# Kernel optimization log

Hardware: AMD Instinct MI355X
Metric: run time of the kernel (lower is better)

The kernel has to match this reference:

```python
import jax, jax.numpy as jnp
import numpy as np

B, N, E = 4096, 32, 64
IN_DIM, H = 74, 256
ADD_DIM = 2
MLP1, MLP2 = 1024, 512
GCR_LAYERS = 5


def setup_inputs() -> dict:
    key = jax.random.key(0)
    ks = jax.random.split(key, 26)
    s = 0.05
    inp = {
        "x": jax.random.normal(ks[0], (B, N, IN_DIM), jnp.float32),
        "add_features": jax.random.normal(ks[1], (B, ADD_DIM), jnp.float32),
        "src": jax.random.randint(ks[2], (B, E), 0, N, jnp.int32),
        "dst": jax.random.randint(ks[3], (B, E), 0, N, jnp.int32),
        # first GraphConv (in_dim -> hidden)
        "W_in": jax.random.normal(ks[4], (IN_DIM, H), jnp.float32) * s,
        "b_in": jnp.zeros((H,), jnp.float32),
        # 5 GCR blocks, each with two GraphConv layers (hidden -> hidden)
        "W_g1": jax.random.normal(ks[5], (GCR_LAYERS, H, H), jnp.float32) * s,
        "b_g1": jnp.zeros((GCR_LAYERS, H), jnp.float32),
        "W_g2": jax.random.normal(ks[6], (GCR_LAYERS, H, H), jnp.float32) * s,
        "b_g2": jnp.zeros((GCR_LAYERS, H), jnp.float32),
        # attention pooling
        "Wq": jax.random.normal(ks[7], (H, H), jnp.float32) * s,
        "bq": jnp.zeros((H,), jnp.float32),
        "Wk": jax.random.normal(ks[8], (H, H), jnp.float32) * s,
        "bk": jnp.zeros((H,), jnp.float32),
        "Wv": jax.random.normal(ks[9], (H, 1), jnp.float32) * s,
        "bv": jnp.zeros((1,), jnp.float32),
        "W_m1": jax.random.normal(ks[10], (H + ADD_DIM, MLP1), jnp.float32) * s,
        "b_m1": jnp.zeros((MLP1,), jnp.float32),
        "W_m2": jax.random.normal(ks[11], (MLP1, MLP2), jnp.float32) * s,
        "b_m2": jnp.zeros((MLP2,), jnp.float32),
        "W_m3": jax.random.normal(ks[12], (MLP2, 1), jnp.float32) * s,
        "b_m3": jnp.zeros((1,), jnp.float32),
    }
    return inp


def _forward(x, add_features, src, dst, W_in, b_in, W_g1, b_g1, W_g2, b_g2,
             Wq, bq, Wk, bk, Wv, bv, W_m1, b_m1, W_m2, b_m2, W_m3, b_m3):
    def per_graph(xg, sg, dg):
        # DGL GraphConv norm='both': D_out^{-1/2} on src side, D_in^{-1/2} on dst side
        ones = jnp.ones((E,), xg.dtype)
        out_deg = jnp.zeros((N,), xg.dtype).at[sg].add(ones)
        in_deg = jnp.zeros((N,), xg.dtype).at[dg].add(ones)
        onorm = jax.lax.rsqrt(jnp.clip(out_deg, 1.0))
        inorm = jax.lax.rsqrt(jnp.clip(in_deg, 1.0))

        def conv(h, W, b):
            h = (h * onorm[:, None]) @ W                      # [N, out]
            agg = jnp.zeros((N, W.shape[1]), h.dtype).at[dg].add(h[sg])
            return agg * inorm[:, None] + b

        h = conv(xg, W_in, b_in)
        for i in range(GCR_LAYERS):
            t = conv(h, W_g1[i], b_g1[i])
            t = conv(jax.nn.relu(t), W_g2[i], b_g2[i])
            h = jax.nn.relu(t)                                # GCR output (res_connection=0)
        # attention-weighted pooling over nodes
        q = h @ Wq + bq                                       # [N, H]
        k = h @ Wk + bk                                       # [N, H]
        v = h @ Wv + bv                                       # [N, 1]
        attn = jax.nn.softmax(q @ k.T, axis=1)                # [N, N]
        w = (attn @ v)[:, 0]                                  # [N]
        return h.T @ w                                        # [H]

    feats = jax.vmap(per_graph)(x, src, dst)                  # [B, H]
    z = jnp.concatenate([feats, add_features], axis=1)        # [B, H+ADD_DIM]
    z = jax.nn.leaky_relu(z @ W_m1 + b_m1)
    z = jax.nn.leaky_relu(z @ W_m2 + b_m2)
    z = z @ W_m3 + b_m3                                       # [B, 1]
    return z[:, 0]


def reference(x, add_features, src, dst, W_in, b_in, W_g1, b_g1, W_g2, b_g2,
              Wq, bq, Wk, bk, Wv, bv, W_m1, b_m1, W_m2, b_m2, W_m3, b_m3):
    return _forward(x, add_features, src, dst, W_in, b_in, W_g1, b_g1, W_g2, b_g2,
                    Wq, bq, Wk, bk, Wv, bv, W_m1, b_m1, W_m2, b_m2, W_m3, b_m3)
```

## Files before the change

kernel.cpp:

```cpp
#include <hip/hip_runtime.h>
#include <math.h>

#define BB     4096
#define NN     32
#define EE     64
#define INDIM  74
#define HH     256
#define GCR    5
#define M1     1024
#define M2     512
#define FDIM   258
#define ADDD   2
#define FSTR   288

typedef __attribute__((ext_vector_type(8))) _Float16 half8_t;
typedef __attribute__((ext_vector_type(4))) float float4_t;

#define MF16(a, b, c) __builtin_amdgcn_mfma_f32_16x16x32_f16((a), (b), (c), 0, 0, 0)
#define LO_SCALE 1024.0f

#define WS_FH     0
#define WS_WQK    4227072
#define WS_TVEC   4489216
#define WS_PK     4490240
#define PK_WIN_HI 0
#define PK_WIN_LO 24576
#define PK_G_BASE 49152
#define PK_G_STRIDE 131072
#define PK_WQK_HI 1359872
#define PK_WQK_LO (1359872 + 65536)
#define PK_W1P    1490944
#define PK_W2P    1785856

union H4 { unsigned long long u; _Float16 h[4]; };

__global__ void prep1_kernel(const float* __restrict__ Wq, const float* __restrict__ Wk,
                             const float* __restrict__ bq,
                             float* __restrict__ wqkf, float* __restrict__ tvec) {
  const int i = blockIdx.x, j = threadIdx.x;
  if (i < 256) {
    __shared__ float qrow[256];
    qrow[j] = Wq[i * 256 + j];
    __syncthreads();
    float s = 0.f;
    for (int c = 0; c < 256; ++c) s = fmaf(qrow[c], Wk[j * 256 + c], s);
    wqkf[i * 256 + j] = s;
  } else {
    float s = 0.f;
    for (int c = 0; c < 256; ++c) s = fmaf(Wk[j * 256 + c], bq[c], s);
    tvec[j] = s;
  }
}

template<int KS, int KREAL>
__device__ __forceinline__ void pack_one(const float* __restrict__ S,
                                         _Float16* __restrict__ hi,
                                         _Float16* __restrict__ lo, int local) {
  const int l = local & 63;
  const int nk = local >> 6;
  const int ks = nk % KS;
  const int nt = nk / KS;
  const int j = nt * 16 + (l & 15);
  const int kbase = ks * 32 + (l >> 4) * 8;
  half8_t h8, l8;
  #pragma unroll
  for (int i = 0; i < 8; ++i) {
    const int k = kbase + i;
    const float v = (k < KREAL) ? S[k * 256 + j] : 0.f;
    const _Float16 hb = (_Float16)v;
    h8[i] = hb;
    l8[i] = (_Float16)((v - (float)hb) * LO_SCALE);
  }
  *(half8_t*)(hi + (size_t)local * 8) = h8;
  *(half8_t*)(lo + (size_t)local * 8) = l8;
}

__global__ void prep2_kernel(const float* __restrict__ W_in,
                             const float* __restrict__ W_g1, const float* __restrict__ W_g2,
                             const float* __restrict__ wqkf, _Float16* __restrict__ pk) {
  const int cid = blockIdx.x * 256 + threadIdx.x;
  if (cid < 3072) {
    pack_one<3, 74>(W_in, pk + PK_WIN_HI, pk + PK_WIN_LO, cid);
  } else {
    const int m = (cid - 3072) >> 13;
    const int local = (cid - 3072) & 8191;
    _Float16* hi; const float* S;
    if (m < 10) {
      hi = pk + PK_G_BASE + (size_t)m * PK_G_STRIDE;
      S = (m < 5) ? (W_g1 + (size_t)m * 65536) : (W_g2 + (size_t)(m - 5) * 65536);
    } else {
      hi = pk + PK_WQK_HI;
      S = wqkf;
    }
    pack_one<8, 256>(S, hi, hi + 65536, local);
  }
}

template<int KS, int KREAL, int NCOL>
__device__ __forceinline__ void pack_flat(const float* __restrict__ S,
                                          _Float16* __restrict__ dst, int local) {
  const int l = local & 63;
  const int nk = local >> 6;
  const int ks = nk % KS;
  const int nt = nk / KS;
  const int j = nt * 16 + (l & 15);
  const int kbase = ks * 32 + (l >> 4) * 8;
  half8_t h8;
  #pragma unroll
  for (int i = 0; i < 8; ++i) {
    const int k = kbase + i;
    h8[i] = (_Float16)((k < KREAL) ? S[(size_t)k * NCOL + j] : 0.f);
  }
  *(half8_t*)(dst + (size_t)local * 8) = h8;
}

__global__ void prep3_kernel(const float* __restrict__ W1, const float* __restrict__ W2,
                             _Float16* __restrict__ pk) {
  const int cid = blockIdx.x * 256 + threadIdx.x;
  if (cid < 36864) {
    pack_flat<9, 258, 1024>(W1, pk + PK_W1P, cid);
  } else {
    pack_flat<32, 1024, 512>(W2, pk + PK_W2P, cid - 36864);
  }
}

template<int KS, bool RELU>
__device__ __forceinline__ void conv2x(
    _Float16* Hs, _Float16* Tb,
    const half8_t nm[2][2],
    const _Float16* __restrict__ Whi,
    const float* __restrict__ bias,
    int lane, int wv)
{
  const int g4 = lane >> 4, l15 = lane & 15;
  const int sw = l15 << 3;

  float4_t th[2][2][2];
  #pragma unroll
  for (int a = 0; a < 2; ++a)
    #pragma unroll
    for (int b = 0; b < 2; ++b)
      #pragma unroll
      for (int c = 0; c < 2; ++c)
        th[a][b][c] = (float4_t){0.f, 0.f, 0.f, 0.f};

  #pragma unroll
  for (int ks = 0; ks < KS; ++ks) {
    const half8_t wh0 = *(const half8_t*)(Whi + ((wv * KS + ks) * 64 + lane) * 8);
    const half8_t wh1 = *(const half8_t*)(Whi + (((8 + wv) * KS + ks) * 64 + lane) * 8);
    const int j0 = ks * 32 + g4 * 8;
    #pragma unroll
    for (int gi = 0; gi < 2; ++gi)
      #pragma unroll
      for (int mt = 0; mt < 2; ++mt) {
        const half8_t ha = *(const half8_t*)(Hs + (gi << 13) + ((mt * 16 + l15) * 256 + (j0 ^ sw)));
        th[0][gi][mt] = MF16(ha, wh0, th[0][gi][mt]);
        th[1][gi][mt] = MF16(ha, wh1, th[1][gi][mt]);
      }
  }

  #pragma unroll
  for (int ni = 0; ni < 2; ++ni) {
    const int nt = ni * 8 + wv;
    #pragma unroll
    for (int gi = 0; gi < 2; ++gi)
      #pragma unroll
      for (int mt = 0; mt < 2; ++mt) {
        const int r0 = mt * 16 + 4 * g4;
        H4 pk4;
        #pragma unroll
        for (int jj = 0; jj < 4; ++jj)
          pk4.h[jj] = (_Float16)th[ni][gi][mt][jj];
        const int idx = nt * 512 + ((r0 >> 3) * 16 + l15) * 8 + (r0 & 7);
        *(unsigned long long*)(Tb + (gi << 13) + idx) = pk4.u;
      }
  }

  __syncthreads();

  #pragma unroll
  for (int ni = 0; ni < 2; ++ni) {
    const int nt = ni * 8 + wv;
    const float4 b4 = *(const float4*)&bias[nt * 16 + 4 * g4];
    const int j0 = nt * 16 + 4 * g4;
    #pragma unroll
    for (int gi = 0; gi < 2; ++gi) {
      const half8_t ta = *(const half8_t*)(Tb + (gi << 13) + nt * 512 + lane * 8);
      #pragma unroll
      for (int nt2 = 0; nt2 < 2; ++nt2) {
        const float4_t dh = MF16(ta, nm[gi][nt2], ((float4_t){0.f, 0.f, 0.f, 0.f}));
        H4 pk4;
        #pragma unroll
        for (int jj = 0; jj < 4; ++jj) {
          float v = dh[jj] + ((const float*)&b4)[jj];
          if (RELU) v = fmaxf(v, 0.f);
          pk4.h[jj] = (_Float16)v;
        }
        const int n = nt2 * 16 + l15;
        *(unsigned long long*)(Hs + (gi << 13) + (n * 256 + (j0 ^ ((n & 15) << 3)))) = pk4.u;
      }
    }
  }
  __syncthreads();
}

__global__ __launch_bounds__(512, 4)
void gnn_kernel(const float* __restrict__ x, const float* __restrict__ addf,
                const int* __restrict__ src, const int* __restrict__ dst,
                const float* __restrict__ b_in,
                const float* __restrict__ b_g1, const float* __restrict__ b_g2,
                const float* __restrict__ Wvp, const float* __restrict__ bv,
                const _Float16* __restrict__ pk,
                const float* __restrict__ tvec,
                _Float16* __restrict__ Fh)
{
  __shared__ __align__(16) _Float16 Hs[2][8192];
  __shared__ __align__(16) _Float16 Tb[2][8192];
  __shared__ float Sb[2][1184];

  const int tid = threadIdx.x;
  const int lane = tid & 63;
  const int wv = tid >> 6;
  const int g4 = lane >> 4, l15 = lane & 15;
  const int sw = l15 << 3;
  const int ga = blockIdx.x * 2;

  for (int i = tid; i < 2048; i += 512) Sb[i >> 10][i & 1023] = 0.f;
  __syncthreads();
  if (tid < 128) {
    const int gi = tid >> 6, e = tid & 63;
    const int es = src[(size_t)(ga + gi) * EE + e];
    const int ed = dst[(size_t)(ga + gi) * EE + e];
    atomicAdd(&Sb[gi][ed * 32 + es], 1.0f);
  }
  __syncthreads();
  if (tid < 64) {
    const int gi = tid >> 5, n = tid & 31;
    float s = 0.f;
    for (int m = 0; m < NN; ++m) s += Sb[gi][n * 32 + m];
    Sb[gi][1056 + n] = 1.f / sqrtf(fmaxf(s, 1.f));
  } else if (tid < 128) {
    const int gi = (tid - 64) >> 5, n = tid & 31;
    float s = 0.f;
    for (int m = 0; m < NN; ++m) s += Sb[gi][m * 32 + n];
    Sb[gi][1088 + n] = 1.f / sqrtf(fmaxf(s, 1.f));
  }
  __syncthreads();
  for (int i = tid; i < 2048; i += 512) {
    const int gi = i >> 10, idx = i & 1023;
    Sb[gi][idx] *= Sb[gi][1056 + (idx >> 5)] * Sb[gi][1088 + (idx & 31)];
  }
  __syncthreads();

  half8_t nm[2][2];
  #pragma unroll
  for (int gi = 0; gi < 2; ++gi)
    #pragma unroll
    for (int nt2 = 0; nt2 < 2; ++nt2)
      #pragma unroll
      for (int i = 0; i < 8; ++i)
        nm[gi][nt2][i] = (_Float16)Sb[gi][(nt2 * 16 + l15) * 32 + g4 * 8 + i];

  for (int i = tid; i < 2 * NN * 96; i += 512) {
    const int gi = i / 3072, rem = i - gi * 3072;
    const int r = rem / 96, c = rem - r * 96;
    const float vx = (c < INDIM) ? x[(size_t)(ga + gi) * (NN * INDIM) + r * INDIM + c] : 0.f;
    Hs[gi][r * 256 + (c ^ ((r & 15) << 3))] = (_Float16)vx;
  }
  __syncthreads();

  conv2x<3, false>(&Hs[0][0], &Tb[0][0], nm, pk + PK_WIN_HI, b_in, lane, wv);
  #pragma unroll 1
  for (int L = 0; L < GCR; ++L) {
    conv2x<8, true>(&Hs[0][0], &Tb[0][0], nm,
                    pk + PK_G_BASE + (size_t)L * PK_G_STRIDE, b_g1 + L * HH, lane, wv);
    conv2x<8, true>(&Hs[0][0], &Tb[0][0], nm,
                    pk + PK_G_BASE + (size_t)(5 + L) * PK_G_STRIDE, b_g2 + L * HH, lane, wv);
  }

  {
    const _Float16* Qhi = pk + PK_WQK_HI;
    const int sgi = wv >> 2, smt = (wv >> 1) & 1, snt = wv & 1;

    float4_t uh[2][2][2];
    #pragma unroll
    for (int a = 0; a < 2; ++a)
      #pragma unroll
      for (int b = 0; b < 2; ++b)
        #pragma unroll
        for (int c = 0; c < 2; ++c)
          uh[a][b][c] = (float4_t){0.f, 0.f, 0.f, 0.f};

    #pragma unroll
    for (int ks = 0; ks < 8; ++ks) {
      const half8_t qh0 = *(const half8_t*)(Qhi + ((wv * 8 + ks) * 64 + lane) * 8);
      const half8_t qh1 = *(const half8_t*)(Qhi + (((8 + wv) * 8 + ks) * 64 + lane) * 8);
      const int j0 = ks * 32 + g4 * 8;
      #pragma unroll
      for (int gi = 0; gi < 2; ++gi)
        #pragma unroll
        for (int mt = 0; mt < 2; ++mt) {
          const half8_t ha = *(const half8_t*)(&Hs[gi][(mt * 16 + l15) * 256 + (j0 ^ sw)]);
          uh[0][gi][mt] = MF16(ha, qh0, uh[0][gi][mt]);
          uh[1][gi][mt] = MF16(ha, qh1, uh[1][gi][mt]);
        }
    }
    #pragma unroll
    for (int ni = 0; ni < 2; ++ni) {
      const int nt = ni * 8 + wv;
      const float tv = tvec[nt * 16 + l15];
      const int cl = nt * 16 + l15;
      #pragma unroll
      for (int gi = 0; gi < 2; ++gi)
        #pragma unroll
        for (int mt = 0; mt < 2; ++mt)
          #pragma unroll
          for (int jj = 0; jj < 4; ++jj) {
            const int n = mt * 16 + 4 * g4 + jj;
            Tb[gi][n * 256 + (cl ^ ((n & 15) << 3))] =
                (_Float16)(uh[ni][gi][mt][jj] + tv);
          }
    }
    __syncthreads();
    float4_t sacc = (float4_t){0.f, 0.f, 0.f, 0.f};
    #pragma unroll
    for (int ksl = 0; ksl < 8; ++ksl) {
      const int kl = ksl * 32 + g4 * 8;
      const half8_t ua = *(const half8_t*)(&Tb[sgi][(smt * 16 + l15) * 256 + (kl ^ sw)]);
      const half8_t hb = *(const half8_t*)(&Hs[sgi][(snt * 16 + l15) * 256 + (kl ^ sw)]);
      sacc = MF16(ua, hb, sacc);
    }
    #pragma unroll
    for (int jj = 0; jj < 4; ++jj)
      Sb[sgi][(smt * 16 + 4 * g4 + jj) * 33 + snt * 16 + l15] = sacc[jj];
  }

  {
    const int gi = tid >> 8, m = (tid >> 3) & 31, q = tid & 7;
    float s = 0.f;
    const int c0 = q * 32;
    for (int cc = 0; cc < 32; ++cc) {
      const int c = c0 + cc;
      s = fmaf((float)Hs[gi][m * 256 + (c ^ ((m & 15) << 3))], Wvp[c], s);
    }
    s += __shfl_xor(s, 1);
    s += __shfl_xor(s, 2);
    s += __shfl_xor(s, 4);
    if (q == 0) Sb[gi][1120 + m] = s + bv[0];
  }
  __syncthreads();

  if (tid < 64) {
    const int gi = tid >> 5, n = tid & 31;
    float mx = -1e30f;
    #pragma unroll 1
    for (int m = 0; m < NN; ++m) mx = fmaxf(mx, Sb[gi][n * 33 + m]);
    float se = 0.f, sv = 0.f;
    #pragma unroll 1
    for (int m = 0; m < NN; ++m) {
      const float e = expf(Sb[gi][n * 33 + m] - mx);
      se += e;
      sv = fmaf(e, Sb[gi][1120 + m], sv);
    }
    Sb[gi][1152 + n] = sv / se;
  }
  __syncthreads();

  {
    const int gi = tid >> 8, j = tid & 255;
    float f0 = 0.f;
    #pragma unroll
    for (int m = 0; m < NN; ++m) {
      const float w = Sb[gi][1152 + m];
      f0 = fmaf((float)Hs[gi][m * 256 + (j ^ ((m & 15) << 3))], w, f0);
    }
    Fh[(size_t)(ga + gi) * FSTR + j] = (_Float16)f0;
    if (tid < 64) {
      const int g2 = tid >> 5, c = 256 + (tid & 31);
      Fh[(size_t)(ga + g2) * FSTR + c] =
          (c < FDIM) ? (_Float16)addf[(size_t)(ga + g2) * ADDD + (c - 256)] : (_Float16)0.f;
    }
  }
}

__global__ __launch_bounds__(512, 4)
void mlp_kernel(const _Float16* __restrict__ Fh,
                const _Float16* __restrict__ W1p, const float* __restrict__ b1,
                const _Float16* __restrict__ W2p, const float* __restrict__ b2,
                const float* __restrict__ W3, const float* __restrict__ b3,
                float* __restrict__ out)
{
  __shared__ __align__(16) _Float16 Ft[16 * 320];
  __shared__ __align__(16) _Float16 Z1[16 * 1024];
  __shared__ __align__(16) _Float16 Z2[16 * 512];

  const int tid = threadIdx.x, lane = tid & 63, wv = tid >> 6;
  const int g4 = lane >> 4, l15 = lane & 15;
  const int sw = (l15 & 7) << 3;
  const int r0 = blockIdx.x * 16;

  for (int i = tid; i < 16 * FSTR; i += 512) {
    const int r = i / FSTR, c = i - r * FSTR;
    Ft[r * 320 + (c ^ ((r & 7) << 3))] = Fh[(size_t)(r0 + r) * FSTR + c];
  }
  __syncthreads();

  {
    float4_t a1[8];
    #pragma unroll
    for (int t = 0; t < 8; ++t) a1[t] = (float4_t){0.f, 0.f, 0.f, 0.f};
    #pragma unroll
    for (int ks = 0; ks < 9; ++ks) {
      const half8_t fb = *(const half8_t*)(Ft + l15 * 320 + ((ks * 32 + g4 * 8) ^ sw));
      #pragma unroll
      for (int t = 0; t < 8; ++t) {
        const int jt = wv * 8 + t;
        const half8_t wf = *(const half8_t*)(W1p + ((size_t)(jt * 9 + ks) * 64 + lane) * 8);
        a1[t] = MF16(wf, fb, a1[t]);
      }
    }
    #pragma unroll
    for (int t = 0; t < 8; ++t) {
      const int j0 = (wv * 8 + t) * 16 + 4 * g4;
      const float4 bb = *(const float4*)&b1[j0];
      H4 pk4;
      #pragma unroll
      for (int jj = 0; jj < 4; ++jj) {
        const float z = a1[t][jj] + ((const float*)&bb)[jj];
        pk4.h[jj] = (_Float16)fmaxf(z, 0.01f * z);
      }
      *(unsigned long long*)(Z1 + l15 * 1024 + (j0 ^ sw)) = pk4.u;
    }
  }
  __syncthreads();

  {
    float4_t a2[4];
    #pragma unroll
    for (int t = 0; t < 4; ++t) a2[t] = (float4_t){0.f, 0.f, 0.f, 0.f};
    #pragma unroll 4
    for (int ks = 0; ks < 32; ++ks) {
      const half8_t zb = *(const half8_t*)(Z1 + l15 * 1024 + ((ks * 32 + g4 * 8) ^ sw));
      #pragma unroll
      for (int t = 0; t < 4; ++t) {
        const int jt = wv * 4 + t;
        const half8_t wf = *(const half8_t*)(W2p + ((size_t)(jt * 32 + ks) * 64 + lane) * 8);
        a2[t] = MF16(wf, zb, a2[t]);
      }
    }
    #pragma unroll
    for (int t = 0; t < 4; ++t) {
      const int j0 = (wv * 4 + t) * 16 + 4 * g4;
      const float4 bb = *(const float4*)&b2[j0];
      H4 pk4;
      #pragma unroll
      for (int jj = 0; jj < 4; ++jj) {
        const float z = a2[t][jj] + ((const float*)&bb)[jj];
        pk4.h[jj] = (_Float16)fmaxf(z, 0.01f * z);
      }
      *(unsigned long long*)(Z2 + l15 * 512 + (j0 ^ sw)) = pk4.u;
    }
  }
  __syncthreads();

  {
    const int m = tid >> 5, q = tid & 31;
    const int swm = (m & 7) << 3;
    float s = 0.f;
    #pragma unroll
    for (int h = 0; h < 2; ++h) {
      const int c0 = q * 16 + h * 8;
      const half8_t z8 = *(const half8_t*)(Z2 + m * 512 + (c0 ^ swm));
      #pragma unroll
      for (int i2 = 0; i2 < 8; ++i2)
        s = fmaf((float)z8[i2], W3[c0 + i2], s);
    }
    s += __shfl_xor(s, 1);
    s += __shfl_xor(s, 2);
    s += __shfl_xor(s, 4);
    s += __shfl_xor(s, 8);
    s += __shfl_xor(s, 16);
    if (q == 0) out[r0 + m] = s + b3[0];
  }
}

extern "C" void kernel_launch(void* const* d_in, const int* in_sizes, int n_in,
                              void* d_out, int out_size, void* d_ws, size_t ws_size,
                              hipStream_t stream) {
  (void)in_sizes; (void)n_in; (void)out_size; (void)ws_size;
  const float* x    = (const float*)d_in[0];
  const float* addf = (const float*)d_in[1];
  const int*   src  = (const int*)d_in[2];
  const int*   dst  = (const int*)d_in[3];
  const float* W_in = (const float*)d_in[4];
  const float* b_in = (const float*)d_in[5];
  const float* W_g1 = (const float*)d_in[6];
  const float* b_g1 = (const float*)d_in[7];
  const float* W_g2 = (const float*)d_in[8];
  const float* b_g2 = (const float*)d_in[9];
  const float* Wq   = (const float*)d_in[10];
  const float* bq   = (const float*)d_in[11];
  const float* Wk   = (const float*)d_in[12];
  const float* Wv   = (const float*)d_in[14];
  const float* bv   = (const float*)d_in[15];
  const float* W1   = (const float*)d_in[16];
  const float* b1   = (const float*)d_in[17];
  const float* W2   = (const float*)d_in[18];
  const float* b2   = (const float*)d_in[19];
  const float* W3   = (const float*)d_in[20];
  const float* b3   = (const float*)d_in[21];
  float* out = (float*)d_out;

  _Float16* Fh    = (_Float16*)((char*)d_ws + WS_FH);
  float* wqkf     = (float*)((char*)d_ws + WS_WQK);
  float* tvec     = (float*)((char*)d_ws + WS_TVEC);
  _Float16* pk    = (_Float16*)((char*)d_ws + WS_PK);

  prep1_kernel<<<dim3(257), dim3(256), 0, stream>>>(Wq, Wk, bq, wqkf, tvec);
  prep2_kernel<<<dim3(364), dim3(256), 0, stream>>>(W_in, W_g1, W_g2, wqkf, pk);
  prep3_kernel<<<dim3(400), dim3(256), 0, stream>>>(W1, W2, pk);
  gnn_kernel<<<dim3(BB / 2), dim3(512), 0, stream>>>(
      x, addf, src, dst, b_in, b_g1, b_g2, Wv, bv, pk, tvec, Fh);
  mlp_kernel<<<dim3(BB / 16), dim3(512), 0, stream>>>(
      Fh, pk + PK_W1P, b1, pk + PK_W2P, b2, W3, b3, out);
}
```

Before: 341.4 us.

## Switch GNN conv layers to 32x32x16 MFMA with per-wave column tiles

Rewrites the graph-conv and Q·K projection stages to use 32x32x16 f16 MFMA, so each wave owns a 32-column slice across all 32 nodes instead of two 16-column tiles. The weight packing is changed to match the new fragment layout, and the unused lo-part packing is dropped. The aggregation step now uses per-wave transposed scratch with a new swizzle. The aim is fewer MFMA issues and LDS fragment loads per layer. In exchange, accumulator register pressure rises, and the new LDS swizzles could introduce bank conflicts.

```diff
diff --git a/kernel.cpp b/kernel.cpp
--- a/kernel.cpp
+++ b/kernel.cpp
@@ -15,24 +15,30 @@
 
 typedef __attribute__((ext_vector_type(8))) _Float16 half8_t;
 typedef __attribute__((ext_vector_type(4))) float float4_t;
+typedef __attribute__((ext_vector_type(16))) float float16_t;
 
 #define MF16(a, b, c) __builtin_amdgcn_mfma_f32_16x16x32_f16((a), (b), (c), 0, 0, 0)
-#define LO_SCALE 1024.0f
+#define MF32(a, b, c) __builtin_amdgcn_mfma_f32_32x32x16_f16((a), (b), (c), 0, 0, 0)
 
 #define WS_FH     0
 #define WS_WQK    4227072
 #define WS_TVEC   4489216
 #define WS_PK     4490240
 #define PK_WIN_HI 0
-#define PK_WIN_LO 24576
 #define PK_G_BASE 49152
 #define PK_G_STRIDE 131072
 #define PK_WQK_HI 1359872
-#define PK_WQK_LO (1359872 + 65536)
 #define PK_W1P    1490944
 #define PK_W2P    1785856
 
 union H4 { unsigned long long u; _Float16 h[4]; };
+
+__device__ __forceinline__ float16_t zero16() {
+  float16_t z;
+  #pragma unroll
+  for (int e = 0; e < 16; ++e) z[e] = 0.f;
+  return z;
+}
 
 __global__ void prep1_kernel(const float* __restrict__ Wq, const float* __restrict__ Wk,
                              const float* __restrict__ bq,
@@ -52,27 +58,22 @@
   }
 }
 
-template<int KS, int KREAL>
-__device__ __forceinline__ void pack_one(const float* __restrict__ S,
-                                         _Float16* __restrict__ hi,
-                                         _Float16* __restrict__ lo, int local) {
+template<int KS16, int KREAL>
+__device__ __forceinline__ void pack32(const float* __restrict__ S,
+                                       _Float16* __restrict__ dst, int local) {
   const int l = local & 63;
   const int nk = local >> 6;
-  const int ks = nk % KS;
-  const int nt = nk / KS;
-  const int j = nt * 16 + (l & 15);
-  const int kbase = ks * 32 + (l >> 4) * 8;
-  half8_t h8, l8;
+  const int ks = nk % KS16;
+  const int nt = nk / KS16;
+  const int j = nt * 32 + (l & 31);
+  const int kbase = ks * 16 + (l >> 5) * 8;
+  half8_t h8;
   #pragma unroll
   for (int i = 0; i < 8; ++i) {
     const int k = kbase + i;
-    const float v = (k < KREAL) ? S[k * 256 + j] : 0.f;
-    const _Float16 hb = (_Float16)v;
-    h8[i] = hb;
-    l8[i] = (_Float16)((v - (float)hb) * LO_SCALE);
-  }
-  *(half8_t*)(hi + (size_t)local * 8) = h8;
-  *(half8_t*)(lo + (size_t)local * 8) = l8;
+    h8[i] = (_Float16)((k < KREAL) ? S[k * 256 + j] : 0.f);
+  }
+  *(half8_t*)(dst + (size_t)local * 8) = h8;
 }
 
 __global__ void prep2_kernel(const float* __restrict__ W_in,
@@ -80,19 +81,16 @@
                              const float* __restrict__ wqkf, _Float16* __restrict__ pk) {
   const int cid = blockIdx.x * 256 + threadIdx.x;
   if (cid < 3072) {
-    pack_one<3, 74>(W_in, pk + PK_WIN_HI, pk + PK_WIN_LO, cid);
+    pack32<6, 74>(W_in, pk + PK_WIN_HI, cid);
   } else {
     const int m = (cid - 3072) >> 13;
     const int local = (cid - 3072) & 8191;
-    _Float16* hi; const float* S;
     if (m < 10) {
-      hi = pk + PK_G_BASE + (size_t)m * PK_G_STRIDE;
-      S = (m < 5) ? (W_g1 + (size_t)m * 65536) : (W_g2 + (size_t)(m - 5) * 65536);
+      const float* S = (m < 5) ? (W_g1 + (size_t)m * 65536) : (W_g2 + (size_t)(m - 5) * 65536);
+      pack32<16, 256>(S, pk + PK_G_BASE + (size_t)m * PK_G_STRIDE, local);
     } else {
-      hi = pk + PK_WQK_HI;
-      S = wqkf;
-    }
-    pack_one<8, 256>(S, hi, hi + 65536, local);
+      pack32<16, 256>(wqkf, pk + PK_WQK_HI, local);
+    }
   }
 }
 
@@ -124,82 +122,68 @@
   }
 }
 
-template<int KS, bool RELU>
-__device__ __forceinline__ void conv2x(
-    _Float16* Hs, _Float16* Tb,
-    const half8_t nm[2][2],
-    const _Float16* __restrict__ Whi,
-    const float* __restrict__ bias,
+template<int KS16, bool RELU>
+__device__ __forceinline__ void conv32(
+    _Float16* Hs, _Float16* Tb, const half8_t nm[2][2],
+    const _Float16* __restrict__ Whi, const float* __restrict__ bias,
     int lane, int wv)
 {
-  const int g4 = lane >> 4, l15 = lane & 15;
-  const int sw = l15 << 3;
-
-  float4_t th[2][2][2];
-  #pragma unroll
-  for (int a = 0; a < 2; ++a)
-    #pragma unroll
-    for (int b = 0; b < 2; ++b)
-      #pragma unroll
-      for (int c = 0; c < 2; ++c)
-        th[a][b][c] = (float4_t){0.f, 0.f, 0.f, 0.f};
-
-  #pragma unroll
-  for (int ks = 0; ks < KS; ++ks) {
-    const half8_t wh0 = *(const half8_t*)(Whi + ((wv * KS + ks) * 64 + lane) * 8);
-    const half8_t wh1 = *(const half8_t*)(Whi + (((8 + wv) * KS + ks) * 64 + lane) * 8);
-    const int j0 = ks * 32 + g4 * 8;
-    #pragma unroll
-    for (int gi = 0; gi < 2; ++gi)
-      #pragma unroll
-      for (int mt = 0; mt < 2; ++mt) {
-        const half8_t ha = *(const half8_t*)(Hs + (gi << 13) + ((mt * 16 + l15) * 256 + (j0 ^ sw)));
-        th[0][gi][mt] = MF16(ha, wh0, th[0][gi][mt]);
-        th[1][gi][mt] = MF16(ha, wh1, th[1][gi][mt]);
-      }
-  }
-
-  #pragma unroll
-  for (int ni = 0; ni < 2; ++ni) {
-    const int nt = ni * 8 + wv;
-    #pragma unroll
-    for (int gi = 0; gi < 2; ++gi)
-      #pragma unroll
-      for (int mt = 0; mt < 2; ++mt) {
-        const int r0 = mt * 16 + 4 * g4;
-        H4 pk4;
-        #pragma unroll
-        for (int jj = 0; jj < 4; ++jj)
-          pk4.h[jj] = (_Float16)th[ni][gi][mt][jj];
-        const int idx = nt * 512 + ((r0 >> 3) * 16 + l15) * 8 + (r0 & 7);
-        *(unsigned long long*)(Tb + (gi << 13) + idx) = pk4.u;
-      }
-  }
-
-  __syncthreads();
-
-  #pragma unroll
-  for (int ni = 0; ni < 2; ++ni) {
-    const int nt = ni * 8 + wv;
-    const float4 b4 = *(const float4*)&bias[nt * 16 + 4 * g4];
-    const int j0 = nt * 16 + 4 * g4;
-    #pragma unroll
-    for (int gi = 0; gi < 2; ++gi) {
-      const half8_t ta = *(const half8_t*)(Tb + (gi << 13) + nt * 512 + lane * 8);
-      #pragma unroll
-      for (int nt2 = 0; nt2 < 2; ++nt2) {
-        const float4_t dh = MF16(ta, nm[gi][nt2], ((float4_t){0.f, 0.f, 0.f, 0.f}));
-        H4 pk4;
-        #pragma unroll
-        for (int jj = 0; jj < 4; ++jj) {
-          float v = dh[jj] + ((const float*)&b4)[jj];
-          if (RELU) v = fmaxf(v, 0.f);
-          pk4.h[jj] = (_Float16)v;
-        }
-        const int n = nt2 * 16 + l15;
-        *(unsigned long long*)(Hs + (gi << 13) + (n * 256 + (j0 ^ ((n & 15) << 3)))) = pk4.u;
-      }
-    }
+  const int r31 = lane & 31, g2 = lane >> 5;
+  const int swA = (r31 & 15) << 3;
+  _Float16* Tw0 = Tb + wv * 1024;
+  _Float16* Tw1 = Tb + 8192 + wv * 1024;
+
+  float16_t acc0 = zero16(), acc1 = zero16();
+  #pragma unroll 4
+  for (int ks = 0; ks < KS16; ++ks) {
+    const half8_t wh = *(const half8_t*)(Whi + ((size_t)(wv * KS16 + ks) * 64 + lane) * 8);
+    const int k0 = ks * 16 + g2 * 8;
+    const half8_t ha0 = *(const half8_t*)(Hs + (r31 * 256 + (k0 ^ swA)));
+    const half8_t ha1 = *(const half8_t*)(Hs + 8192 + (r31 * 256 + (k0 ^ swA)));
+    acc0 = MF32(ha0, wh, acc0);
+    acc1 = MF32(ha1, wh, acc1);
+  }
+  const int swT = (r31 & 3) << 3;
+  #pragma unroll
+  for (int q = 0; q < 4; ++q) {
+    const int n0 = 8 * q + 4 * g2;
+    H4 p0, p1;
+    #pragma unroll
+    for (int jj = 0; jj < 4; ++jj) {
+      p0.h[jj] = (_Float16)acc0[4 * q + jj];
+      p1.h[jj] = (_Float16)acc1[4 * q + jj];
+    }
+    *(unsigned long long*)(Tw0 + r31 * 32 + (n0 ^ swT)) = p0.u;
+    *(unsigned long long*)(Tw1 + r31 * 32 + (n0 ^ swT)) = p1.u;
+  }
+
+  __syncthreads();
+
+  float16_t d0 = zero16(), d1 = zero16();
+  #pragma unroll
+  for (int ks2 = 0; ks2 < 2; ++ks2) {
+    const int n0 = ks2 * 16 + g2 * 8;
+    const half8_t t0 = *(const half8_t*)(Tw0 + r31 * 32 + (n0 ^ swT));
+    const half8_t t1 = *(const half8_t*)(Tw1 + r31 * 32 + (n0 ^ swT));
+    d0 = MF32(t0, nm[0][ks2], d0);
+    d1 = MF32(t1, nm[1][ks2], d1);
+  }
+  const int swn = (r31 & 15) << 3;
+  #pragma unroll
+  for (int q = 0; q < 4; ++q) {
+    const int j0 = wv * 32 + 8 * q + 4 * g2;
+    const float4 bb = *(const float4*)&bias[j0];
+    H4 p0, p1;
+    #pragma unroll
+    for (int jj = 0; jj < 4; ++jj) {
+      float v0 = d0[4 * q + jj] + ((const float*)&bb)[jj];
+      float v1 = d1[4 * q + jj] + ((const float*)&bb)[jj];
+      if (RELU) { v0 = fmaxf(v0, 0.f); v1 = fmaxf(v1, 0.f); }
+      p0.h[jj] = (_Float16)v0;
+      p1.h[jj] = (_Float16)v1;
+    }
+    *(unsigned long long*)(Hs + (r31 * 256 + (j0 ^ swn))) = p0.u;
+    *(unsigned long long*)(Hs + 8192 + (r31 * 256 + (j0 ^ swn))) = p1.u;
   }
   __syncthreads();
 }
@@ -221,8 +205,9 @@
   const int tid = threadIdx.x;
   const int lane = tid & 63;
   const int wv = tid >> 6;
+  const int r31 = lane & 31, g2 = lane >> 5;
   const int g4 = lane >> 4, l15 = lane & 15;
-  const int sw = l15 << 3;
+  const int swA = (r31 & 15) << 3;
   const int ga = blockIdx.x * 2;
 
   for (int i = tid; i < 2048; i += 512) Sb[i >> 10][i & 1023] = 0.f;
@@ -256,10 +241,10 @@
   #pragma unroll
   for (int gi = 0; gi < 2; ++gi)
     #pragma unroll
-    for (int nt2 = 0; nt2 < 2; ++nt2)
+    for (int ks2 = 0; ks2 < 2; ++ks2)
       #pragma unroll
       for (int i = 0; i < 8; ++i)
-        nm[gi][nt2][i] = (_Float16)Sb[gi][(nt2 * 16 + l15) * 32 + g4 * 8 + i];
+        nm[gi][ks2][i] = (_Float16)Sb[gi][r31 * 32 + ks2 * 16 + g2 * 8 + i];
 
   for (int i = tid; i < 2 * NN * 96; i += 512) {
     const int gi = i / 3072, rem = i - gi * 3072;
@@ -269,59 +254,47 @@
   }
   __syncthreads();
 
-  conv2x<3, false>(&Hs[0][0], &Tb[0][0], nm, pk + PK_WIN_HI, b_in, lane, wv);
+  conv32<6, false>(&Hs[0][0], &Tb[0][0], nm, pk + PK_WIN_HI, b_in, lane, wv);
   #pragma unroll 1
   for (int L = 0; L < GCR; ++L) {
-    conv2x<8, true>(&Hs[0][0], &Tb[0][0], nm,
-                    pk + PK_G_BASE + (size_t)L * PK_G_STRIDE, b_g1 + L * HH, lane, wv);
-    conv2x<8, true>(&Hs[0][0], &Tb[0][0], nm,
-                    pk + PK_G_BASE + (size_t)(5 + L) * PK_G_STRIDE, b_g2 + L * HH, lane, wv);
-  }
-
-  {
-    const _Float16* Qhi = pk + PK_WQK_HI;
+    conv32<16, true>(&Hs[0][0], &Tb[0][0], nm,
+                     pk + PK_G_BASE + (size_t)L * PK_G_STRIDE, b_g1 + L * HH, lane, wv);
+    conv32<16, true>(&Hs[0][0], &Tb[0][0], nm,
+                     pk + PK_G_BASE + (size_t)(5 + L) * PK_G_STRIDE, b_g2 + L * HH, lane, wv);
+  }
+
+  {
+    const _Float16* Qp = pk + PK_WQK_HI;
+    float16_t ua0 = zero16(), ua1 = zero16();
+    #pragma unroll 4
+    for (int ks = 0; ks < 16; ++ks) {
+      const half8_t qf = *(const half8_t*)(Qp + ((size_t)(wv * 16 + ks) * 64 + lane) * 8);
+      const int k0 = ks * 16 + g2 * 8;
+      const half8_t hb0 = *(const half8_t*)(&Hs[0][r31 * 256 + (k0 ^ swA)]);
+      const half8_t hb1 = *(const half8_t*)(&Hs[1][r31 * 256 + (k0 ^ swA)]);
+      ua0 = MF32(qf, hb0, ua0);
+      ua1 = MF32(qf, hb1, ua1);
+    }
+    const int swn = (r31 & 15) << 3;
+    #pragma unroll
+    for (int q = 0; q < 4; ++q) {
+      const int j0 = wv * 32 + 8 * q + 4 * g2;
+      const float4 tv = *(const float4*)&tvec[j0];
+      H4 p0, p1;
+      #pragma unroll
+      for (int jj = 0; jj < 4; ++jj) {
+        p0.h[jj] = (_Float16)(ua0[4 * q + jj] + ((const float*)&tv)[jj]);
+        p1.h[jj] = (_Float16)(ua1[4 * q + jj] + ((const float*)&tv)[jj]);
+      }
+      *(unsigned long long*)(&Tb[0][r31 * 256 + (j0 ^ swn)]) = p0.u;
+      *(unsigned long long*)(&Tb[1][r31 * 256 + (j0 ^ swn)]) = p1.u;
+    }
+  }
+  __syncthreads();
+
+  {
     const int sgi = wv >> 2, smt = (wv >> 1) & 1, snt = wv & 1;
-
-    float4_t uh[2][2][2];
-    #pragma unroll
-    for (int a = 0; a < 2; ++a)
-      #pragma unroll
-      for (int b = 0; b < 2; ++b)
-        #pragma unroll
-        for (int c = 0; c < 2; ++c)
-          uh[a][b][c] = (float4_t){0.f, 0.f, 0.f, 0.f};
-
-    #pragma unroll
-    for (int ks = 0; ks < 8; ++ks) {
-      const half8_t qh0 = *(const half8_t*)(Qhi + ((wv * 8 + ks) * 64 + lane) * 8);
-      const half8_t qh1 = *(const half8_t*)(Qhi + (((8 + wv) * 8 + ks) * 64 + lane) * 8);
-      const int j0 = ks * 32 + g4 * 8;
-      #pragma unroll
-      for (int gi = 0; gi < 2; ++gi)
-        #pragma unroll
-        for (int mt = 0; mt < 2; ++mt) {
-          const half8_t ha = *(const half8_t*)(&Hs[gi][(mt * 16 + l15) * 256 + (j0 ^ sw)]);
-          uh[0][gi][mt] = MF16(ha, qh0, uh[0][gi][mt]);
-          uh[1][gi][mt] = MF16(ha, qh1, uh[1][gi][mt]);
-        }
-    }
-    #pragma unroll
-    for (int ni = 0; ni < 2; ++ni) {
-      const int nt = ni * 8 + wv;
-      const float tv = tvec[nt * 16 + l15];
-      const int cl = nt * 16 + l15;
-      #pragma unroll
-      for (int gi = 0; gi < 2; ++gi)
-        #pragma unroll
-        for (int mt = 0; mt < 2; ++mt)
-          #pragma unroll
-          for (int jj = 0; jj < 4; ++jj) {
-            const int n = mt * 16 + 4 * g4 + jj;
-            Tb[gi][n * 256 + (cl ^ ((n & 15) << 3))] =
-                (_Float16)(uh[ni][gi][mt][jj] + tv);
-          }
-    }
-    __syncthreads();
+    const int sw = l15 << 3;
     float4_t sacc = (float4_t){0.f, 0.f, 0.f, 0.f};
     #pragma unroll
     for (int ksl = 0; ksl < 8; ++ksl) {
@@ -332,7 +305,7 @@
     }
     #pragma unroll
     for (int jj = 0; jj < 4; ++jj)
-      Sb[sgi][(smt * 16 + 4 * g4 + jj) * 33 + snt * 16 + l15] = sacc[jj];
+      Sb[sgi][(smt * 16 + 4 * (g4 & 3) + jj) * 33 + snt * 16 + l15] = sacc[jj];
   }
 
   {
@@ -376,9 +349,9 @@
     }
     Fh[(size_t)(ga + gi) * FSTR + j] = (_Float16)f0;
     if (tid < 64) {
-      const int g2 = tid >> 5, c = 256 + (tid & 31);
-      Fh[(size_t)(ga + g2) * FSTR + c] =
-          (c < FDIM) ? (_Float16)addf[(size_t)(ga + g2) * ADDD + (c - 256)] : (_Float16)0.f;
+      const int g2b = tid >> 5, c = 256 + (tid & 31);
+      Fh[(size_t)(ga + g2b) * FSTR + c] =
+          (c < FDIM) ? (_Float16)addf[(size_t)(ga + g2b) * ADDD + (c - 256)] : (_Float16)0.f;
     }
   }
 }
```

New measurement: 361.3 us. 5.8% more time.
